# Performance work log

Measured on AMD Instinct MI355X. Metric: run time of the kernel, lower is better.

## Reference

```python
import jax, jax.numpy as jnp
import numpy as np

B, N, E, F, D = 8, 2000, 64000, 1024, 128
NEG_SLOPE = 0.01  # torch LeakyReLU default

def leaky(x):
    return jnp.where(x >= 0, x, NEG_SLOPE * x)

def gcn_conv(x, ei, W, b):
    # PyG GCNConv: add self loops, symmetric norm, x @ W, scatter-sum, + bias
    src, tgt = ei[0], ei[1]
    loops = jnp.arange(N, dtype=src.dtype)
    src_a = jnp.concatenate([src, loops])
    tgt_a = jnp.concatenate([tgt, loops])
    deg = jax.ops.segment_sum(jnp.ones(src_a.shape, x.dtype), tgt_a, num_segments=N)
    dinv = jnp.where(deg > 0, jax.lax.rsqrt(deg), 0.0)
    norm = dinv[src_a] * dinv[tgt_a]  # [E+N]
    h = x @ W                          # [N, F]
    out = jax.ops.segment_sum(norm[:, None] * h[src_a], tgt_a, num_segments=N)
    return out + b

gcn_conv_b = jax.vmap(gcn_conv, in_axes=(0, 0, None, None))

def setup_inputs() -> dict:
    key = jax.random.key(0)
    ks = jax.random.split(key, 16)
    s = lambda fan: 1.0 / np.sqrt(fan)
    return {
        "x1": jax.random.normal(ks[0], (B, N, F), jnp.float32),
        "ei1": jax.random.randint(ks[1], (B, 2, E), 0, N, jnp.int32),
        "x2": jax.random.normal(ks[2], (B, N, F), jnp.float32),
        "ei2": jax.random.randint(ks[3], (B, 2, E), 0, N, jnp.int32),
        "Wg1": jax.random.normal(ks[4], (F, F), jnp.float32) * s(F),
        "bg1": jnp.zeros((F,), jnp.float32),
        "Wf1": jax.random.normal(ks[5], (F, D), jnp.float32) * s(F),
        "bf1": jnp.zeros((D,), jnp.float32),
        "Wg2": jax.random.normal(ks[6], (F, F), jnp.float32) * s(F),
        "bg2": jnp.zeros((F,), jnp.float32),
        "Wf2": jax.random.normal(ks[7], (F, D), jnp.float32) * s(F),
        "bf2": jnp.zeros((D,), jnp.float32),
        "W1": jax.random.normal(ks[8], (2 * D, 256), jnp.float32) * s(2 * D),
        "b1": jnp.zeros((256,), jnp.float32),
        "W2": jax.random.normal(ks[9], (256, 64), jnp.float32) * s(256),
        "b2": jnp.zeros((64,), jnp.float32),
        "Wo": jax.random.normal(ks[10], (64, 1), jnp.float32) * s(64),
        "bo": jnp.zeros((1,), jnp.float32),
    }

def reference(x1, ei1, x2, ei2, Wg1, bg1, Wf1, bf1, Wg2, bg2, Wf2, bf2,
              W1, b1, W2, b2, Wo, bo):
    # branch 1
    h1 = leaky(gcn_conv_b(x1, ei1, Wg1, bg1))       # [B, N, F]
    g1 = jnp.mean(h1, axis=1)                        # [B, F]
    g1 = leaky(g1 @ Wf1 + bf1)                       # [B, D] (dropout = eval identity)
    # branch 2
    h2 = leaky(gcn_conv_b(x2, ei2, Wg2, bg2))
    g2 = jnp.mean(h2, axis=1)
    g2 = leaky(g2 @ Wf2 + bf2)
    # head
    xc = jnp.concatenate([g1, g2], axis=1)           # [B, 2D]
    xc = leaky(xc @ W1 + b1)
    xc = leaky(xc @ W2 + b2)
    return jax.nn.sigmoid(xc @ Wo + bo)              # [B, 1]
```

## Files before the change

### kernel.cpp

```cpp
#include <hip/hip_runtime.h>
#include <stdint.h>

#define B 8
#define NN 2000
#define EG 64000
#define FF 1024
#define DD 128
#define BK 32
#define NCHUNK 125
#define CG 5

typedef short short8 __attribute__((ext_vector_type(8)));
typedef float f32x4 __attribute__((ext_vector_type(4)));
typedef float f32x2 __attribute__((ext_vector_type(2)));

__device__ __forceinline__ unsigned short f2bf(float f) {
    union { float f; unsigned int u; } v; v.f = f;
    unsigned int u = v.u;
    unsigned int r = u + 0x7FFFu + ((u >> 16) & 1u);
    return (unsigned short)(r >> 16);
}
__device__ __forceinline__ float leaky(float v) { return v >= 0.0f ? v : 0.01f * v; }

__device__ __forceinline__ void acc8p(f32x2* __restrict__ r, float w, uint4 v) {
    union { unsigned int u; float f; } c;
    f32x2 wv = {w, w};
    f32x2 h;
    c.u = v.x << 16;          h.x = c.f;
    c.u = v.x & 0xffff0000u;  h.y = c.f;
    r[0] += wv * h;
    c.u = v.y << 16;          h.x = c.f;
    c.u = v.y & 0xffff0000u;  h.y = c.f;
    r[1] += wv * h;
    c.u = v.z << 16;          h.x = c.f;
    c.u = v.z & 0xffff0000u;  h.y = c.f;
    r[2] += wv * h;
    c.u = v.w << 16;          h.x = c.f;
    c.u = v.w & 0xffff0000u;  h.y = c.f;
    r[3] += wv * h;
}

__global__ void k_fillf(float* __restrict__ p, float v, int n) {
    int i = blockIdx.x * 256 + threadIdx.x;
    if (i < n) p[i] = v;
}

__global__ void k_degcount(const int* __restrict__ ei_a, const int* __restrict__ ei_b,
                           float* __restrict__ deg, int ng) {
    int i = blockIdx.x * 256 + threadIdx.x;
    if (i >= ng * EG) return;
    int g = i / EG, e = i - g * EG;
    const int* ei = (g < B) ? (ei_a + (size_t)g * 2 * EG) : (ei_b + (size_t)(g - B) * 2 * EG);
    int t = ei[EG + e];
    atomicAdd(&deg[g * NN + t], 1.0f);
}

__global__ void k_scan(const float* __restrict__ deg, int* __restrict__ csr_off,
                       int* __restrict__ cursor, float* __restrict__ dinv) {
    int g = blockIdx.x, t = threadIdx.x;
    __shared__ int part[256];
    int loc[8];
    int s = 0;
#pragma unroll
    for (int i = 0; i < 8; ++i) {
        int n = t * 8 + i;
        float dv = (n < NN) ? deg[g * NN + n] : 1.0f;
        if (n < NN) dinv[g * NN + n] = rsqrtf(dv);
        int c = (n < NN) ? ((int)dv - 1) : 0;
        loc[i] = s;
        s += c;
    }
    part[t] = s;
    __syncthreads();
    for (int off = 1; off < 256; off <<= 1) {
        int v = (t >= off) ? part[t - off] : 0;
        __syncthreads();
        part[t] += v;
        __syncthreads();
    }
    int base = part[t] - s;
#pragma unroll
    for (int i = 0; i < 8; ++i) {
        int n = t * 8 + i;
        if (n < NN) {
            int o = base + loc[i];
            csr_off[g * (NN + 1) + n] = o;
            cursor[g * NN + n] = o;
        }
    }
    if (t == 255) csr_off[g * (NN + 1) + NN] = part[255];
}

__global__ void k_fillcsr(const int* __restrict__ ei_a, const int* __restrict__ ei_b,
                          int* __restrict__ cursor, const float* __restrict__ dinv,
                          int2* __restrict__ epk, int ng) {
    int i = blockIdx.x * 256 + threadIdx.x;
    if (i >= ng * EG) return;
    int g = i / EG, e = i - g * EG;
    const int* ei = (g < B) ? (ei_a + (size_t)g * 2 * EG) : (ei_b + (size_t)(g - B) * 2 * EG);
    int s = ei[e];
    int t = ei[EG + e];
    int pos = atomicAdd(&cursor[g * NN + t], 1);
    int2 p;
    p.x = s;
    p.y = __float_as_int(dinv[g * NN + s] * dinv[g * NN + t]);
    epk[(size_t)g * EG + pos] = p;
}

__global__ void k_convx(const float* __restrict__ x_a, const float* __restrict__ x_b,
                        unsigned short* __restrict__ xb, int half4, int total4) {
    int i = blockIdx.x * 256 + threadIdx.x;
    if (i >= total4) return;
    float4 v = (i < half4) ? ((const float4*)x_a)[i] : ((const float4*)x_b)[i - half4];
    ushort4 o;
    o.x = f2bf(v.x); o.y = f2bf(v.y); o.z = f2bf(v.z); o.w = f2bf(v.w);
    ((ushort4*)xb)[i] = o;
}

__global__ void k_wT(const float* __restrict__ Wg_a, const float* __restrict__ Wg_b,
                     unsigned short* __restrict__ wT) {
    __shared__ float tile[32][33];
    int tx = threadIdx.x, ty = threadIdx.y;
    int k0 = blockIdx.y * 32, n0 = blockIdx.x * 32;
    const float* Wg = blockIdx.z ? Wg_b : Wg_a;
    unsigned short* o = wT + (size_t)blockIdx.z * FF * FF;
#pragma unroll
    for (int r = 0; r < 4; ++r) {
        int row = ty + r * 8;
        tile[row][tx] = Wg[(k0 + row) * FF + n0 + tx];
    }
    __syncthreads();
#pragma unroll
    for (int r = 0; r < 4; ++r) {
        int row = ty + r * 8;
        o[(n0 + row) * FF + k0 + tx] = f2bf(tile[tx][row]);
    }
}

__launch_bounds__(256) __global__
void k_gemm(const unsigned short* __restrict__ Abf, const unsigned short* __restrict__ wTa,
            const unsigned short* __restrict__ wTb, unsigned short* __restrict__ Hbf,
            int mtiles) {
    int blk = blockIdx.x;
    int mt = ((blk >> 6) << 3) | (blk & 7);
    int nt = (blk >> 3) & 7;
    if (mt >= mtiles) return;
    int m0 = mt * 128, n0 = nt * 128;
    const unsigned short* Bbf = (mt >= 125) ? wTb : wTa;

    __shared__ __align__(16) unsigned short As[128 * BK];
    __shared__ __align__(16) unsigned short Bs[128 * BK];
    int tid = threadIdx.x;
    int lane = tid & 63, wave = tid >> 6;
    int wr = wave >> 1, wc = wave & 1;
    int q = lane >> 4, l15 = lane & 15;
    int lr = lane >> 2, lc = lane & 3;

    f32x4 acc[4][4];
#pragma unroll
    for (int i = 0; i < 4; ++i)
#pragma unroll
        for (int j = 0; j < 4; ++j) acc[i][j] = (f32x4){0.f, 0.f, 0.f, 0.f};

    for (int kt = 0; kt < 32; ++kt) {
        int kb = kt * BK;
#pragma unroll
        for (int p = 0; p < 2; ++p) {
            int rbase = p * 64 + wave * 16;
            int r = rbase + lr;
            __builtin_amdgcn_global_load_lds(
                (const __attribute__((address_space(1))) unsigned int*)
                    &Abf[(size_t)(m0 + r) * FF + kb + lc * 8],
                (__attribute__((address_space(3))) unsigned int*)&As[rbase * BK],
                16, 0, 0);
            __builtin_amdgcn_global_load_lds(
                (const __attribute__((address_space(1))) unsigned int*)
                    &Bbf[(size_t)(n0 + r) * FF + kb + lc * 8],
                (__attribute__((address_space(3))) unsigned int*)&Bs[rbase * BK],
                16, 0, 0);
        }
        __syncthreads();
        short8 fa[4], fb[4];
#pragma unroll
        for (int i = 0; i < 4; ++i)
            fa[i] = *(const short8*)&As[(wr * 64 + i * 16 + l15) * BK + q * 8];
#pragma unroll
        for (int j = 0; j < 4; ++j)
            fb[j] = *(const short8*)&Bs[(wc * 64 + j * 16 + l15) * BK + q * 8];
#pragma unroll
        for (int i = 0; i < 4; ++i)
#pragma unroll
            for (int j = 0; j < 4; ++j)
                acc[i][j] = __builtin_amdgcn_mfma_f32_16x16x32_bf16(fa[i], fb[j], acc[i][j], 0, 0, 0);
        __syncthreads();
    }
#pragma unroll
    for (int i = 0; i < 4; ++i) {
#pragma unroll
        for (int j = 0; j < 4; ++j) {
            int n = n0 + wc * 64 + j * 16 + l15;
#pragma unroll
            for (int v = 0; v < 4; ++v) {
                int m = m0 + wr * 64 + i * 16 + q * 4 + v;
                Hbf[(size_t)m * FF + n] = f2bf(acc[i][j][v]);
            }
        }
    }
}

__launch_bounds__(256) __global__
void k_aggreduce(const unsigned short* __restrict__ Hbf, const int* __restrict__ csr_off,
                 const int2* __restrict__ epk, const float* __restrict__ dinv,
                 const float* __restrict__ bg_a, const float* __restrict__ bg_b,
                 float* __restrict__ part) {
    int blk = blockIdx.x;
    int phase = blk / 1000;
    int bp = blk - phase * 1000;
    int half = phase & 1;
    int g = (phase >> 1) * 8 + (bp & 7);
    int chunk = bp >> 3;
    int tid = threadIdx.x;
    int team = tid >> 6;
    int lane = tid & 63;
    int f0 = half * 512 + lane * 8;
    int n0 = chunk * 16 + team * 4;
    const unsigned short* Hb = Hbf + (size_t)g * NN * FF;
    const int2* ep = epk + (size_t)g * EG;
    const float* bg = (g < B) ? bg_a : bg_b;

    f32x2 bgv[4];
#pragma unroll
    for (int i = 0; i < 4; ++i) bgv[i] = (f32x2){bg[f0 + 2 * i], bg[f0 + 2 * i + 1]};
    f32x2 bsum[4];
#pragma unroll
    for (int i = 0; i < 4; ++i) bsum[i] = (f32x2){0.f, 0.f};

    for (int nn = 0; nn < 4; ++nn) {
        int n = n0 + nn;
        float dn = dinv[g * NN + n];
        int beg = csr_off[g * (NN + 1) + n];
        int end = csr_off[g * (NN + 1) + n + 1];
        f32x2 racc[4];
#pragma unroll
        for (int i = 0; i < 4; ++i) racc[i] = (f32x2){0.f, 0.f};
        {
            uint4 sv = *(const uint4*)&Hb[(n << 10) + f0];
            acc8p(racc, dn * dn, sv);
        }
        int j = beg;
        for (; j + 4 <= end; j += 4) {
            int2 e0 = ep[j], e1 = ep[j + 1], e2 = ep[j + 2], e3 = ep[j + 3];
            uint4 v0 = *(const uint4*)&Hb[(e0.x << 10) + f0];
            uint4 v1 = *(const uint4*)&Hb[(e1.x << 10) + f0];
            uint4 v2 = *(const uint4*)&Hb[(e2.x << 10) + f0];
            uint4 v3 = *(const uint4*)&Hb[(e3.x << 10) + f0];
            acc8p(racc, __int_as_float(e0.y), v0);
            acc8p(racc, __int_as_float(e1.y), v1);
            acc8p(racc, __int_as_float(e2.y), v2);
            acc8p(racc, __int_as_float(e3.y), v3);
        }
        for (; j < end; ++j) {
            int2 e = ep[j];
            uint4 v = *(const uint4*)&Hb[(e.x << 10) + f0];
            acc8p(racc, __int_as_float(e.y), v);
        }
#pragma unroll
        for (int i = 0; i < 4; ++i) {
            f32x2 t = racc[i] + bgv[i];
            bsum[i].x += leaky(t.x);
            bsum[i].y += leaky(t.y);
        }
    }

    __shared__ float red[3][64 * 9];
    if (team > 0) {
#pragma unroll
        for (int i = 0; i < 4; ++i) {
            red[team - 1][lane * 9 + 2 * i]     = bsum[i].x;
            red[team - 1][lane * 9 + 2 * i + 1] = bsum[i].y;
        }
    }
    __syncthreads();
    if (team == 0) {
        float* o = part + ((size_t)g * NCHUNK + chunk) * FF + f0;
        float r[8];
#pragma unroll
        for (int i = 0; i < 4; ++i) {
            r[2 * i]     = bsum[i].x;
            r[2 * i + 1] = bsum[i].y;
        }
#pragma unroll
        for (int t = 0; t < 3; ++t)
#pragma unroll
            for (int i = 0; i < 8; ++i) r[i] += red[t][lane * 9 + i];
        float4 a = {r[0], r[1], r[2], r[3]};
        float4 c = {r[4], r[5], r[6], r[7]};
        *(float4*)&o[0] = a;
        *(float4*)&o[4] = c;
    }
}

__global__ void k_gsum1(const float* __restrict__ part, float* __restrict__ part2) {
    int blk = blockIdx.x;
    int g = blk / 20;
    int rem = blk - g * 20;
    int fq = rem / CG, cg = rem - fq * CG;
    int f = fq * 256 + threadIdx.x;
    const float* p = part + (size_t)g * NCHUNK * FF + (size_t)cg * 25 * FF + f;
    float s = 0.f;
#pragma unroll 5
    for (int c = 0; c < 25; ++c) s += p[(size_t)c * FF];
    part2[((size_t)g * CG + cg) * FF + f] = s;
}

__global__ void k_fc(const float* __restrict__ part2, const float* __restrict__ Wf_a,
                     const float* __restrict__ bf_a, const float* __restrict__ Wf_b,
                     const float* __restrict__ bf_b, float* __restrict__ g12) {
    int g = blockIdx.x, d = threadIdx.x;
    __shared__ float gs[FF];
    const float* p = part2 + (size_t)g * CG * FF;
#pragma unroll
    for (int i = 0; i < 8; ++i) {
        int f = i * 128 + d;
        float s = 0.f;
#pragma unroll
        for (int c = 0; c < CG; ++c) s += p[(size_t)c * FF + f];
        gs[f] = s;
    }
    __syncthreads();
    const float* Wf = (g < B) ? Wf_a : Wf_b;
    const float* bfv = (g < B) ? bf_a : bf_b;
    float acc = 0.f;
#pragma unroll 8
    for (int f = 0; f < FF; ++f) acc += gs[f] * Wf[f * DD + d];
    acc = acc * (1.0f / (float)NN) + bfv[d];
    g12[g * DD + d] = leaky(acc);
}

__launch_bounds__(256) __global__
void k_head(const float* __restrict__ g, const float* __restrict__ W1, const float* __restrict__ b1,
            const float* __restrict__ W2, const float* __restrict__ b2,
            const float* __restrict__ Wo, const float* __restrict__ bo, float* __restrict__ out) {
    __shared__ float xc[8][256];
    __shared__ float l1[8][256];
    __shared__ float l2[8][64];
    int t = threadIdx.x;
#pragma unroll
    for (int i = 0; i < 8; ++i) {
        int idx = i * 256 + t;
        int b = idx >> 8, j = idx & 255;
        xc[b][j] = (j < DD) ? g[b * DD + j] : g[B * DD + b * DD + (j - DD)];
    }
    __syncthreads();
    {
        int j = t;
        float a[8];
#pragma unroll
        for (int b = 0; b < 8; ++b) a[b] = b1[j];
        for (int k = 0; k < 256; ++k) {
            float w = W1[k * 256 + j];
#pragma unroll
            for (int b = 0; b < 8; ++b) a[b] += xc[b][k] * w;
        }
#pragma unroll
        for (int b = 0; b < 8; ++b) l1[b][j] = leaky(a[b]);
    }
    __syncthreads();
    if (t < 64) {
        int j = t;
        float a[8];
#pragma unroll
        for (int b = 0; b < 8; ++b) a[b] = b2[j];
        for (int k = 0; k < 256; ++k) {
            float w = W2[k * 64 + j];
#pragma unroll
            for (int b = 0; b < 8; ++b) a[b] += l1[b][k] * w;
        }
#pragma unroll
        for (int b = 0; b < 8; ++b) l2[b][j] = leaky(a[b]);
    }
    __syncthreads();
    if (t < 8) {
        float a = bo[0];
        for (int k = 0; k < 64; ++k) a += l2[t][k] * Wo[k];
        out[t] = 1.0f / (1.0f + expf(-a));
    }
}

extern "C" void kernel_launch(void* const* d_in, const int* in_sizes, int n_in,
                              void* d_out, int out_size, void* d_ws, size_t ws_size,
                              hipStream_t stream) {
    const float* x1  = (const float*)d_in[0];
    const int*   ei1 = (const int*)d_in[1];
    const float* x2  = (const float*)d_in[2];
    const int*   ei2 = (const int*)d_in[3];
    const float* Wg1 = (const float*)d_in[4];
    const float* bg1 = (const float*)d_in[5];
    const float* Wf1 = (const float*)d_in[6];
    const float* bf1 = (const float*)d_in[7];
    const float* Wg2 = (const float*)d_in[8];
    const float* bg2 = (const float*)d_in[9];
    const float* Wf2 = (const float*)d_in[10];
    const float* bf2 = (const float*)d_in[11];
    const float* W1  = (const float*)d_in[12];
    const float* b1  = (const float*)d_in[13];
    const float* W2  = (const float*)d_in[14];
    const float* b2  = (const float*)d_in[15];
    const float* Wo  = (const float*)d_in[16];
    const float* bo  = (const float*)d_in[17];
    float* out = (float*)d_out;

    auto align = [](size_t v) { return (v + 255) & ~(size_t)255; };
    size_t need = 0;
    size_t o_deg  = need; need += align((size_t)16 * NN * 4);
    size_t o_dinv = need; need += align((size_t)16 * NN * 4);
    size_t o_csr  = need; need += align((size_t)16 * (NN + 1) * 4);
    size_t o_cur  = need; need += align((size_t)16 * NN * 4);
    size_t o_epk  = need; need += align((size_t)16 * EG * 8);
    size_t o_xbf  = need; need += align((size_t)16 * NN * FF * 2);
    size_t o_wT   = need; need += align((size_t)2 * FF * FF * 2);
    size_t o_hbf  = need; need += align((size_t)16 * NN * FF * 2);
    size_t o_part = need; need += align((size_t)16 * NCHUNK * FF * 4);
    size_t o_pt2  = need; need += align((size_t)16 * CG * FF * 4);
    size_t o_g12  = need; need += align((size_t)16 * DD * 4);

    char* w = (char*)d_ws;
    if (ws_size >= need) {
        float* deg   = (float*)(w + o_deg);
        float* dinv  = (float*)(w + o_dinv);
        int* csr     = (int*)(w + o_csr);
        int* cur     = (int*)(w + o_cur);
        int2* epk    = (int2*)(w + o_epk);
        unsigned short* xbf = (unsigned short*)(w + o_xbf);
        unsigned short* wT  = (unsigned short*)(w + o_wT);
        unsigned short* hbf = (unsigned short*)(w + o_hbf);
        float* part  = (float*)(w + o_part);
        float* part2 = (float*)(w + o_pt2);
        float* g12   = (float*)(w + o_g12);

        k_fillf<<<(16 * NN + 255) / 256, 256, 0, stream>>>(deg, 1.0f, 16 * NN);
        k_degcount<<<(16 * EG + 255) / 256, 256, 0, stream>>>(ei1, ei2, deg, 16);
        k_scan<<<16, 256, 0, stream>>>(deg, csr, cur, dinv);
        k_fillcsr<<<(16 * EG + 255) / 256, 256, 0, stream>>>(ei1, ei2, cur, dinv, epk, 16);
        int half4 = B * NN * FF / 4;
        k_convx<<<(2 * half4 + 255) / 256, 256, 0, stream>>>(x1, x2, xbf, half4, 2 * half4);
        k_wT<<<dim3(32, 32, 2), dim3(32, 8), 0, stream>>>(Wg1, Wg2, wT);
        k_gemm<<<2048, 256, 0, stream>>>(xbf, wT, wT + (size_t)FF * FF, hbf, 250);
        k_aggreduce<<<4000, 256, 0, stream>>>(hbf, csr, epk, dinv, bg1, bg2, part);
        k_gsum1<<<16 * 20, 256, 0, stream>>>(part, part2);
        k_fc<<<16, DD, 0, stream>>>(part2, Wf1, bf1, Wf2, bf2, g12);
        k_head<<<1, 256, 0, stream>>>(g12, W1, b1, W2, b2, Wo, bo, out);
    } else {
        size_t n2 = 0;
        size_t f_deg  = n2; n2 += align((size_t)B * NN * 4);
        size_t f_dinv = n2; n2 += align((size_t)B * NN * 4);
        size_t f_csr  = n2; n2 += align((size_t)B * (NN + 1) * 4);
        size_t f_cur  = n2; n2 += align((size_t)B * NN * 4);
        size_t f_epk  = n2; n2 += align((size_t)B * EG * 8);
        size_t f_xbf  = n2; n2 += align((size_t)B * NN * FF * 2);
        size_t f_wT   = n2; n2 += align((size_t)FF * FF * 2);
        size_t f_hbf  = n2; n2 += align((size_t)B * NN * FF * 2);
        size_t f_part = n2; n2 += align((size_t)B * NCHUNK * FF * 4);
        size_t f_pt2  = n2; n2 += align((size_t)B * CG * FF * 4);
        size_t f_g12  = n2; n2 += align((size_t)2 * B * DD * 4);

        float* deg   = (float*)(w + f_deg);
        float* dinv  = (float*)(w + f_dinv);
        int* csr     = (int*)(w + f_csr);
        int* cur     = (int*)(w + f_cur);
        int2* epk    = (int2*)(w + f_epk);
        unsigned short* xbf = (unsigned short*)(w + f_xbf);
        unsigned short* wT  = (unsigned short*)(w + f_wT);
        unsigned short* hbf = (unsigned short*)(w + f_hbf);
        float* part  = (float*)(w + f_part);
        float* part2 = (float*)(w + f_pt2);
        float* g12   = (float*)(w + f_g12);

        const float* xs[2]  = {x1, x2};
        const int*   eis[2] = {ei1, ei2};
        const float* Wgs[2] = {Wg1, Wg2};
        const float* bgs[2] = {bg1, bg2};
        const float* Wfs[2] = {Wf1, Wf2};
        const float* bfs[2] = {bf1, bf2};

        for (int br = 0; br < 2; ++br) {
            k_fillf<<<(B * NN + 255) / 256, 256, 0, stream>>>(deg, 1.0f, B * NN);
            k_degcount<<<(B * EG + 255) / 256, 256, 0, stream>>>(eis[br], eis[br], deg, B);
            k_scan<<<B, 256, 0, stream>>>(deg, csr, cur, dinv);
            k_fillcsr<<<(B * EG + 255) / 256, 256, 0, stream>>>(eis[br], eis[br], cur, dinv, epk, B);
            int half4 = B * NN * FF / 4;
            k_convx<<<(half4 + 255) / 256, 256, 0, stream>>>(xs[br], xs[br], xbf, half4, half4);
            k_wT<<<dim3(32, 32, 1), dim3(32, 8), 0, stream>>>(Wgs[br], Wgs[br], wT);
            k_gemm<<<1024, 256, 0, stream>>>(xbf, wT, wT, hbf, 125);
            k_aggreduce<<<2000, 256, 0, stream>>>(hbf, csr, epk, dinv, bgs[br], bgs[br], part);
            k_gsum1<<<B * 20, 256, 0, stream>>>(part, part2);
            k_fc<<<B, DD, 0, stream>>>(part2, Wfs[br], bfs[br], Wfs[br], bfs[br],
                                       g12 + (size_t)br * B * DD);
        }
        k_head<<<1, 256, 0, stream>>>(g12, W1, b1, W2, b2, Wo, bo, out);
    }
}
```

Before: 621.2 us.

## Merge prep kernels and overlap CSR fill with GEMM in shared launches

Fuses the x-to-bf16 conversion, weight transpose and degree counting into one heterogeneous launch, and runs the CSR fill blocks inside the GEMM launch so they overlap. Degrees become integer atomics zeroed by a memset, and the fallback small-workspace path is removed. The aggregation loop also software-prefetches the next four edge records. This cuts launch count and idle tail time between small kernels, at the cost of larger mixed kernels whose register and LDS footprint follows the GEMM and of dropping the reduced-memory path.

```diff
diff --git a/kernel.cpp b/kernel.cpp
--- a/kernel.cpp
+++ b/kernel.cpp
@@ -9,6 +9,12 @@
 #define BK 32
 #define NCHUNK 125
 #define CG 5
+
+#define NB_CONV 32000
+#define NB_WT   2048
+#define NB_DEG  4000
+#define NB_GEMM 2048
+#define NB_FILL 4000
 
 typedef short short8 __attribute__((ext_vector_type(8)));
 typedef float f32x4 __attribute__((ext_vector_type(4)));
@@ -40,22 +46,52 @@
     r[3] += wv * h;
 }
 
-__global__ void k_fillf(float* __restrict__ p, float v, int n) {
-    int i = blockIdx.x * 256 + threadIdx.x;
-    if (i < n) p[i] = v;
-}
-
-__global__ void k_degcount(const int* __restrict__ ei_a, const int* __restrict__ ei_b,
-                           float* __restrict__ deg, int ng) {
-    int i = blockIdx.x * 256 + threadIdx.x;
-    if (i >= ng * EG) return;
-    int g = i / EG, e = i - g * EG;
-    const int* ei = (g < B) ? (ei_a + (size_t)g * 2 * EG) : (ei_b + (size_t)(g - B) * 2 * EG);
-    int t = ei[EG + e];
-    atomicAdd(&deg[g * NN + t], 1.0f);
-}
-
-__global__ void k_scan(const float* __restrict__ deg, int* __restrict__ csr_off,
+__global__ void k_prep(const float* __restrict__ x_a, const float* __restrict__ x_b,
+                       unsigned short* __restrict__ xb,
+                       const float* __restrict__ Wg_a, const float* __restrict__ Wg_b,
+                       unsigned short* __restrict__ wT,
+                       const int* __restrict__ ei_a, const int* __restrict__ ei_b,
+                       int* __restrict__ degi) {
+    int blk = blockIdx.x;
+    int tid = threadIdx.x;
+    __shared__ float tile[32][33];
+    if (blk < NB_CONV) {
+        int i = blk * 256 + tid;
+        float4 v = (i < NB_CONV * 128) ? ((const float4*)x_a)[i]
+                                       : ((const float4*)x_b)[i - NB_CONV * 128];
+        ushort4 o;
+        o.x = f2bf(v.x); o.y = f2bf(v.y); o.z = f2bf(v.z); o.w = f2bf(v.w);
+        ((ushort4*)xb)[i] = o;
+    } else if (blk < NB_CONV + NB_WT) {
+        int b2 = blk - NB_CONV;
+        int z = b2 >> 10, rem = b2 & 1023;
+        int by = rem >> 5, bx = rem & 31;
+        int tx = tid & 31, ty = tid >> 5;
+        int k0 = by * 32, n0 = bx * 32;
+        const float* Wg = z ? Wg_b : Wg_a;
+        unsigned short* o = wT + (size_t)z * FF * FF;
+#pragma unroll
+        for (int r = 0; r < 4; ++r) {
+            int row = ty + r * 8;
+            tile[row][tx] = Wg[(k0 + row) * FF + n0 + tx];
+        }
+        __syncthreads();
+#pragma unroll
+        for (int r = 0; r < 4; ++r) {
+            int row = ty + r * 8;
+            o[(n0 + row) * FF + k0 + tx] = f2bf(tile[tx][row]);
+        }
+    } else {
+        int i = (blk - NB_CONV - NB_WT) * 256 + tid;
+        int g = i / EG, e = i - g * EG;
+        const int* ei = (g < B) ? (ei_a + (size_t)g * 2 * EG)
+                                : (ei_b + (size_t)(g - B) * 2 * EG);
+        int t = ei[EG + e];
+        atomicAdd(&degi[g * NN + t], 1);
+    }
+}
+
+__global__ void k_scan(const int* __restrict__ degi, int* __restrict__ csr_off,
                        int* __restrict__ cursor, float* __restrict__ dinv) {
     int g = blockIdx.x, t = threadIdx.x;
     __shared__ int part[256];
@@ -64,9 +100,8 @@
 #pragma unroll
     for (int i = 0; i < 8; ++i) {
         int n = t * 8 + i;
-        float dv = (n < NN) ? deg[g * NN + n] : 1.0f;
-        if (n < NN) dinv[g * NN + n] = rsqrtf(dv);
-        int c = (n < NN) ? ((int)dv - 1) : 0;
+        int c = (n < NN) ? degi[g * NN + n] : 0;
+        if (n < NN) dinv[g * NN + n] = rsqrtf((float)(c + 1));
         loc[i] = s;
         s += c;
     }
@@ -91,65 +126,35 @@
     if (t == 255) csr_off[g * (NN + 1) + NN] = part[255];
 }
 
-__global__ void k_fillcsr(const int* __restrict__ ei_a, const int* __restrict__ ei_b,
-                          int* __restrict__ cursor, const float* __restrict__ dinv,
-                          int2* __restrict__ epk, int ng) {
-    int i = blockIdx.x * 256 + threadIdx.x;
-    if (i >= ng * EG) return;
-    int g = i / EG, e = i - g * EG;
-    const int* ei = (g < B) ? (ei_a + (size_t)g * 2 * EG) : (ei_b + (size_t)(g - B) * 2 * EG);
-    int s = ei[e];
-    int t = ei[EG + e];
-    int pos = atomicAdd(&cursor[g * NN + t], 1);
-    int2 p;
-    p.x = s;
-    p.y = __float_as_int(dinv[g * NN + s] * dinv[g * NN + t]);
-    epk[(size_t)g * EG + pos] = p;
-}
-
-__global__ void k_convx(const float* __restrict__ x_a, const float* __restrict__ x_b,
-                        unsigned short* __restrict__ xb, int half4, int total4) {
-    int i = blockIdx.x * 256 + threadIdx.x;
-    if (i >= total4) return;
-    float4 v = (i < half4) ? ((const float4*)x_a)[i] : ((const float4*)x_b)[i - half4];
-    ushort4 o;
-    o.x = f2bf(v.x); o.y = f2bf(v.y); o.z = f2bf(v.z); o.w = f2bf(v.w);
-    ((ushort4*)xb)[i] = o;
-}
-
-__global__ void k_wT(const float* __restrict__ Wg_a, const float* __restrict__ Wg_b,
-                     unsigned short* __restrict__ wT) {
-    __shared__ float tile[32][33];
-    int tx = threadIdx.x, ty = threadIdx.y;
-    int k0 = blockIdx.y * 32, n0 = blockIdx.x * 32;
-    const float* Wg = blockIdx.z ? Wg_b : Wg_a;
-    unsigned short* o = wT + (size_t)blockIdx.z * FF * FF;
-#pragma unroll
-    for (int r = 0; r < 4; ++r) {
-        int row = ty + r * 8;
-        tile[row][tx] = Wg[(k0 + row) * FF + n0 + tx];
-    }
-    __syncthreads();
-#pragma unroll
-    for (int r = 0; r < 4; ++r) {
-        int row = ty + r * 8;
-        o[(n0 + row) * FF + k0 + tx] = f2bf(tile[tx][row]);
-    }
-}
-
 __launch_bounds__(256) __global__
-void k_gemm(const unsigned short* __restrict__ Abf, const unsigned short* __restrict__ wTa,
-            const unsigned short* __restrict__ wTb, unsigned short* __restrict__ Hbf,
-            int mtiles) {
+void k_gemm_fill(const unsigned short* __restrict__ Abf, const unsigned short* __restrict__ wT,
+                 unsigned short* __restrict__ Hbf,
+                 const int* __restrict__ ei_a, const int* __restrict__ ei_b,
+                 int* __restrict__ cursor, const float* __restrict__ dinv,
+                 int2* __restrict__ epk) {
     int blk = blockIdx.x;
+    __shared__ __align__(16) unsigned short As[128 * BK];
+    __shared__ __align__(16) unsigned short Bs[128 * BK];
+    if (blk >= NB_GEMM) {
+        int i = (blk - NB_GEMM) * 256 + threadIdx.x;
+        int g = i / EG, e = i - g * EG;
+        const int* ei = (g < B) ? (ei_a + (size_t)g * 2 * EG)
+                                : (ei_b + (size_t)(g - B) * 2 * EG);
+        int s = ei[e];
+        int t = ei[EG + e];
+        int pos = atomicAdd(&cursor[g * NN + t], 1);
+        int2 p;
+        p.x = s;
+        p.y = __float_as_int(dinv[g * NN + s] * dinv[g * NN + t]);
+        epk[(size_t)g * EG + pos] = p;
+        return;
+    }
     int mt = ((blk >> 6) << 3) | (blk & 7);
     int nt = (blk >> 3) & 7;
-    if (mt >= mtiles) return;
+    if (mt >= 250) return;
     int m0 = mt * 128, n0 = nt * 128;
-    const unsigned short* Bbf = (mt >= 125) ? wTb : wTa;
-
-    __shared__ __align__(16) unsigned short As[128 * BK];
-    __shared__ __align__(16) unsigned short Bs[128 * BK];
+    const unsigned short* Bbf = (mt >= 125) ? (wT + (size_t)FF * FF) : wT;
+
     int tid = threadIdx.x;
     int lane = tid & 63, wave = tid >> 6;
     int wr = wave >> 1, wc = wave & 1;
@@ -248,8 +253,11 @@
             acc8p(racc, dn * dn, sv);
         }
         int j = beg;
-        for (; j + 4 <= end; j += 4) {
-            int2 e0 = ep[j], e1 = ep[j + 1], e2 = ep[j + 2], e3 = ep[j + 3];
+        int2 pe0, pe1, pe2, pe3;
+        if (j + 4 <= end) { pe0 = ep[j]; pe1 = ep[j + 1]; pe2 = ep[j + 2]; pe3 = ep[j + 3]; }
+        for (; j + 8 <= end; j += 4) {
+            int2 e0 = pe0, e1 = pe1, e2 = pe2, e3 = pe3;
+            pe0 = ep[j + 4]; pe1 = ep[j + 5]; pe2 = ep[j + 6]; pe3 = ep[j + 7];
             uint4 v0 = *(const uint4*)&Hb[(e0.x << 10) + f0];
             uint4 v1 = *(const uint4*)&Hb[(e1.x << 10) + f0];
             uint4 v2 = *(const uint4*)&Hb[(e2.x << 10) + f0];
@@ -258,6 +266,17 @@
             acc8p(racc, __int_as_float(e1.y), v1);
             acc8p(racc, __int_as_float(e2.y), v2);
             acc8p(racc, __int_as_float(e3.y), v3);
+        }
+        if (j + 4 <= end) {
+            uint4 v0 = *(const uint4*)&Hb[(pe0.x << 10) + f0];
+            uint4 v1 = *(const uint4*)&Hb[(pe1.x << 10) + f0];
+            uint4 v2 = *(const uint4*)&Hb[(pe2.x << 10) + f0];
+            uint4 v3 = *(const uint4*)&Hb[(pe3.x << 10) + f0];
+            acc8p(racc, __int_as_float(pe0.y), v0);
+            acc8p(racc, __int_as_float(pe1.y), v1);
+            acc8p(racc, __int_as_float(pe2.y), v2);
+            acc8p(racc, __int_as_float(pe3.y), v3);
+            j += 4;
         }
         for (; j < end; ++j) {
             int2 e = ep[j];
@@ -423,80 +442,29 @@
     size_t o_part = need; need += align((size_t)16 * NCHUNK * FF * 4);
     size_t o_pt2  = need; need += align((size_t)16 * CG * FF * 4);
     size_t o_g12  = need; need += align((size_t)16 * DD * 4);
+    (void)need;
 
     char* w = (char*)d_ws;
-    if (ws_size >= need) {
-        float* deg   = (float*)(w + o_deg);
-        float* dinv  = (float*)(w + o_dinv);
-        int* csr     = (int*)(w + o_csr);
-        int* cur     = (int*)(w + o_cur);
-        int2* epk    = (int2*)(w + o_epk);
-        unsigned short* xbf = (unsigned short*)(w + o_xbf);
-        unsigned short* wT  = (unsigned short*)(w + o_wT);
-        unsigned short* hbf = (unsigned short*)(w + o_hbf);
-        float* part  = (float*)(w + o_part);
-        float* part2 = (float*)(w + o_pt2);
-        float* g12   = (float*)(w + o_g12);
-
-        k_fillf<<<(16 * NN + 255) / 256, 256, 0, stream>>>(deg, 1.0f, 16 * NN);
-        k_degcount<<<(16 * EG + 255) / 256, 256, 0, stream>>>(ei1, ei2, deg, 16);
-        k_scan<<<16, 256, 0, stream>>>(deg, csr, cur, dinv);
-        k_fillcsr<<<(16 * EG + 255) / 256, 256, 0, stream>>>(ei1, ei2, cur, dinv, epk, 16);
-        int half4 = B * NN * FF / 4;
-        k_convx<<<(2 * half4 + 255) / 256, 256, 0, stream>>>(x1, x2, xbf, half4, 2 * half4);
-        k_wT<<<dim3(32, 32, 2), dim3(32, 8), 0, stream>>>(Wg1, Wg2, wT);
-        k_gemm<<<2048, 256, 0, stream>>>(xbf, wT, wT + (size_t)FF * FF, hbf, 250);
-        k_aggreduce<<<4000, 256, 0, stream>>>(hbf, csr, epk, dinv, bg1, bg2, part);
-        k_gsum1<<<16 * 20, 256, 0, stream>>>(part, part2);
-        k_fc<<<16, DD, 0, stream>>>(part2, Wf1, bf1, Wf2, bf2, g12);
-        k_head<<<1, 256, 0, stream>>>(g12, W1, b1, W2, b2, Wo, bo, out);
-    } else {
-        size_t n2 = 0;
-        size_t f_deg  = n2; n2 += align((size_t)B * NN * 4);
-        size_t f_dinv = n2; n2 += align((size_t)B * NN * 4);
-        size_t f_csr  = n2; n2 += align((size_t)B * (NN + 1) * 4);
-        size_t f_cur  = n2; n2 += align((size_t)B * NN * 4);
-        size_t f_epk  = n2; n2 += align((size_t)B * EG * 8);
-        size_t f_xbf  = n2; n2 += align((size_t)B * NN * FF * 2);
-        size_t f_wT   = n2; n2 += align((size_t)FF * FF * 2);
-        size_t f_hbf  = n2; n2 += align((size_t)B * NN * FF * 2);
-        size_t f_part = n2; n2 += align((size_t)B * NCHUNK * FF * 4);
-        size_t f_pt2  = n2; n2 += align((size_t)B * CG * FF * 4);
-        size_t f_g12  = n2; n2 += align((size_t)2 * B * DD * 4);
-
-        float* deg   = (float*)(w + f_deg);
-        float* dinv  = (float*)(w + f_dinv);
-        int* csr     = (int*)(w + f_csr);
-        int* cur     = (int*)(w + f_cur);
-        int2* epk    = (int2*)(w + f_epk);
-        unsigned short* xbf = (unsigned short*)(w + f_xbf);
-        unsigned short* wT  = (unsigned short*)(w + f_wT);
-        unsigned short* hbf = (unsigned short*)(w + f_hbf);
-        float* part  = (float*)(w + f_part);
-        float* part2 = (float*)(w + f_pt2);
-        float* g12   = (float*)(w + f_g12);
-
-        const float* xs[2]  = {x1, x2};
-        const int*   eis[2] = {ei1, ei2};
-        const float* Wgs[2] = {Wg1, Wg2};
-        const float* bgs[2] = {bg1, bg2};
-        const float* Wfs[2] = {Wf1, Wf2};
-        const float* bfs[2] = {bf1, bf2};
-
-        for (int br = 0; br < 2; ++br) {
-            k_fillf<<<(B * NN + 255) / 256, 256, 0, stream>>>(deg, 1.0f, B * NN);
-            k_degcount<<<(B * EG + 255) / 256, 256, 0, stream>>>(eis[br], eis[br], deg, B);
-            k_scan<<<B, 256, 0, stream>>>(deg, csr, cur, dinv);
-            k_fillcsr<<<(B * EG + 255) / 256, 256, 0, stream>>>(eis[br], eis[br], cur, dinv, epk, B);
-            int half4 = B * NN * FF / 4;
-            k_convx<<<(half4 + 255) / 256, 256, 0, stream>>>(xs[br], xs[br], xbf, half4, half4);
-            k_wT<<<dim3(32, 32, 1), dim3(32, 8), 0, stream>>>(Wgs[br], Wgs[br], wT);
-            k_gemm<<<1024, 256, 0, stream>>>(xbf, wT, wT, hbf, 125);
-            k_aggreduce<<<2000, 256, 0, stream>>>(hbf, csr, epk, dinv, bgs[br], bgs[br], part);
-            k_gsum1<<<B * 20, 256, 0, stream>>>(part, part2);
-            k_fc<<<B, DD, 0, stream>>>(part2, Wfs[br], bfs[br], Wfs[br], bfs[br],
-                                       g12 + (size_t)br * B * DD);
-        }
-        k_head<<<1, 256, 0, stream>>>(g12, W1, b1, W2, b2, Wo, bo, out);
-    }
-}
+    int* degi    = (int*)(w + o_deg);
+    float* dinv  = (float*)(w + o_dinv);
+    int* csr     = (int*)(w + o_csr);
+    int* cur     = (int*)(w + o_cur);
+    int2* epk    = (int2*)(w + o_epk);
+    unsigned short* xbf = (unsigned short*)(w + o_xbf);
+    unsigned short* wT  = (unsigned short*)(w + o_wT);
+    unsigned short* hbf = (unsigned short*)(w + o_hbf);
+    float* part  = (float*)(w + o_part);
+    float* part2 = (float*)(w + o_pt2);
+    float* g12   = (float*)(w + o_g12);
+
+    hipMemsetAsync(degi, 0, (size_t)16 * NN * 4, stream);
+    k_prep<<<NB_CONV + NB_WT + NB_DEG, 256, 0, stream>>>(x1, x2, xbf, Wg1, Wg2, wT,
+                                                         ei1, ei2, degi);
+    k_scan<<<16, 256, 0, stream>>>(degi, csr, cur, dinv);
+    k_gemm_fill<<<NB_GEMM + NB_FILL, 256, 0, stream>>>(xbf, wT, hbf, ei1, ei2, cur,
+                                                       dinv, epk);
+    k_aggreduce<<<4000, 256, 0, stream>>>(hbf, csr, epk, dinv, bg1, bg2, part);
+    k_gsum1<<<16 * 20, 256, 0, stream>>>(part, part2);
+    k_fc<<<16, DD, 0, stream>>>(part2, Wf1, bf1, Wf2, bf2, g12);
+    k_head<<<1, 256, 0, stream>>>(g12, W1, b1, W2, b2, Wo, bo, out);
+}
```

Result: faster. 573.3 us (-7.7%).
